# Kernel tuning notes

Measured on AMD Instinct MI355X. Metric: run time of the kernel, lower is better.

Reference implementation:

```python
import jax, jax.numpy as jnp
import numpy as np

FS = 3        # filter_size
STRIDE = 2
UPPER_PAD = 1
D_MODEL = 512


def setup_inputs() -> dict:
    key = jax.random.key(0)
    k1, k2, k3, k4 = jax.random.split(key, 4)
    b, h, n, d = 4, 8, 2048, D_MODEL
    nc = n // STRIDE
    layer_query = jax.random.normal(k1, (b, h, n, d), dtype=jnp.float32)
    uncompress_in = jax.random.normal(k2, (b, h, nc, d), dtype=jnp.float32)
    # nn.Linear(d*FS, d): weight (d, d*FS), bias (d,)
    W = jax.random.normal(k3, (d, d * FS), dtype=jnp.float32) * 0.02
    bias = jax.random.normal(k4, (d,), dtype=jnp.float32) * 0.01
    return {"layer_query": layer_query, "uncompress_in": uncompress_in,
            "W": W, "bias": bias, "i": 0}


def reference(layer_query, uncompress_in, W, bias, i):
    b, h, n, d = layer_query.shape
    # einsum('ijac,b->ijcab', u, kron_kernel) with kernel=[1,0,...] followed by
    # flatten(-2,-1) == transpose to (b,h,d,nc) then zero-upsample by STRIDE.
    u = jnp.swapaxes(uncompress_in, -1, -2)                      # (b,h,d,nc)
    nc = u.shape[-1]
    t = jnp.zeros(u.shape + (STRIDE,), u.dtype).at[..., 0].set(u)
    t = t.reshape(b, h, d, nc * STRIDE)                          # (b,h,d,nc*S)
    pad = FS - UPPER_PAD - 1
    t = jnp.pad(t, ((0, 0), (0, 0), (0, 0), (pad, pad)))
    # unfold(-1, FS, 1) then keep first n windows: window w covers t[..., w:w+FS]
    windows = jnp.stack([t[..., k:k + n] for k in range(FS)], axis=-1)  # (b,h,d,n,FS)
    up = jnp.transpose(windows, (0, 1, 3, 4, 2))                 # (b,h,n,FS,d)
    res_connect = up.sum(axis=3) / FS                            # (b,h,n,d)
    flat = up.reshape(b, h, n, FS * d)                           # (b,h,n,FS*d)
    out = jax.nn.relu(jnp.einsum('bhnk,dk->bhnd', flat, W) + bias)
    # dropout p=0.0 -> identity
    return layer_query + out + res_connect
```

## Files before the change

kernel.cpp:

```cpp
#include <hip/hip_runtime.h>
#include <cstdint>

#define NC    1024
#define D     512
#define KTOT  512
#define MTOT  32768
#define BK    64

typedef short  short8  __attribute__((ext_vector_type(8)));
typedef float  floatx4 __attribute__((ext_vector_type(4)));

__device__ inline void gl2lds16(const void* gptr, void* lptr) {
  __builtin_amdgcn_global_load_lds(
      (const __attribute__((address_space(1))) void*)gptr,
      (__attribute__((address_space(3))) void*)lptr,
      16, 0, 0);
}

__device__ inline unsigned short f2bf_rne(float f) {
  union { float f; unsigned u; } x; x.f = f;
  unsigned r = x.u + 0x7fffu + ((x.u >> 16) & 1u);
  return (unsigned short)(r >> 16);
}

__global__ __launch_bounds__(256) void cvt_f32_bf16_all(
    const float* __restrict__ srcU, unsigned short* __restrict__ dstU, int n4U,
    const float* __restrict__ srcW, unsigned short* __restrict__ dstW, int n4W) {
  int i = blockIdx.x * 256 + threadIdx.x;
  const float* src;
  unsigned short* dst;
  int idx;
  if (i < n4U) {
    src = srcU; dst = dstU; idx = i;
  } else {
    idx = i - n4U;
    if (idx >= n4W) return;
    src = srcW; dst = dstW;
  }
  float4 v = ((const float4*)src)[idx];
  ushort4 o;
  o.x = f2bf_rne(v.x); o.y = f2bf_rne(v.y);
  o.z = f2bf_rne(v.z); o.w = f2bf_rne(v.w);
  ((ushort4*)dst)[idx] = o;
}

__global__ __launch_bounds__(256, 2) void fused_uncompress_gemm(
    const unsigned short* __restrict__ Ub,
    const unsigned short* __restrict__ Wb,
    const float* __restrict__ U32,
    const float* __restrict__ LQ,
    const float* __restrict__ bias,
    float* __restrict__ out)
{
  __shared__ __attribute__((aligned(16))) unsigned char smem[129*128 + 192*128];
  unsigned char* smemA = smem;
  unsigned char* smemB = smem + 129*128;

  const int bid   = blockIdx.x;
  const int tileM = ((bid >> 6) << 3) | (bid & 7);
  const int tileN = (bid >> 3) & 7;
  const int r0 = tileM * 128;
  const int n0 = tileN * 64;
  const int tid  = threadIdx.x;
  const int wv   = tid >> 6;
  const int ln   = tid & 63;
  const int quad = ln >> 4;
  const int am   = ln & 15;

  floatx4 acc[2][12];
  #pragma unroll
  for (int rt = 0; rt < 2; ++rt)
    #pragma unroll
    for (int ct = 0; ct < 12; ++ct)
      acc[rt][ct] = floatx4{0.f, 0.f, 0.f, 0.f};

  const bool zeroExtra = (((r0 + 128) & (NC - 1)) == 0);

  for (int kc = 0; kc < KTOT / BK; ++kc) {
    const int k0 = kc * BK;

    #pragma unroll
    for (int i = 0; i < 4; ++i) {
      int row = wv * 32 + i * 8 + (ln >> 3);
      int s   = ln & 7;
      int kch = s ^ (row & 7);
      const unsigned short* g = Ub + (size_t)(r0 + row) * KTOT + k0 + kch * 8;
      gl2lds16(g, smemA + (wv * 32 + i * 8) * 128);
    }
    if (wv == 0 && ln < 8) {
      if (zeroExtra) {
        *(float4*)(smemA + 128 * 128 + ln * 16) = make_float4(0.f, 0.f, 0.f, 0.f);
      } else {
        const unsigned short* g = Ub + (size_t)(r0 + 128) * KTOT + k0 + ln * 8;
        gl2lds16(g, smemA + 128 * 128);
      }
    }
    #pragma unroll
    for (int i = 0; i < 6; ++i) {
      int rho = wv * 48 + i * 8 + (ln >> 3);
      int s   = ln & 7;
      int kch = s ^ (rho & 7);
      int beta = rho >> 6;
      int nl   = rho & 63;
      const unsigned short* g =
          Wb + (size_t)(n0 + nl) * 1536 + beta * 512 + k0 + kch * 8;
      gl2lds16(g, smemB + (wv * 48 + i * 8) * 128);
    }
    __syncthreads();

    #pragma unroll
    for (int ks = 0; ks < 2; ++ks) {
      short8 a0[2], a1[2];
      #pragma unroll
      for (int rt = 0; rt < 2; ++rt) {
        int row  = wv * 32 + rt * 16 + am;
        int sl   = (ks * 4 + quad) ^ (row & 7);
        a0[rt] = *(const short8*)(smemA + row * 128 + sl * 16);
        int row1 = row + 1;
        int sl1  = (ks * 4 + quad) ^ (row1 & 7);
        a1[rt] = *(const short8*)(smemA + row1 * 128 + sl1 * 16);
      }
      #pragma unroll
      for (int ct = 0; ct < 12; ++ct) {
        int beta = ct >> 2;
        int nl   = (ct & 3) * 16 + am;
        int rho  = beta * 64 + nl;
        int sl   = (ks * 4 + quad) ^ (nl & 7);
        short8 b = *(const short8*)(smemB + rho * 128 + sl * 16);
        #pragma unroll
        for (int rt = 0; rt < 2; ++rt) {
          acc[rt][ct] = __builtin_amdgcn_mfma_f32_16x16x32_bf16(
              (beta == 2) ? a1[rt] : a0[rt], b, acc[rt][ct], 0, 0, 0);
        }
      }
    }
    __syncthreads();
  }

  const float inv3 = 1.0f / 3.0f;
  float* Ew = (float*)smem + (size_t)wv * 2 * 16 * 68;
  float* Ow = Ew + 16 * 68;

  #pragma unroll
  for (int rt = 0; rt < 2; ++rt) {
    #pragma unroll
    for (int dt = 0; dt < 4; ++dt) {
      float bv = bias[n0 + dt * 16 + am];
      #pragma unroll
      for (int r = 0; r < 4; ++r) {
        int row16 = quad * 4 + r;
        float p0 = acc[rt][dt][r];
        float p1 = acc[rt][4 + dt][r];
        float p2 = acc[rt][8 + dt][r];
        Ew[row16 * 68 + dt * 16 + am] = fmaxf(p1 + bv, 0.f);
        Ow[row16 * 68 + dt * 16 + am] = fmaxf(p0 + p2 + bv, 0.f);
      }
    }
    #pragma unroll
    for (int rr = 0; rr < 4; ++rr) {
      int row16 = rr * 4 + quad;
      int jl = wv * 32 + rt * 16 + row16;
      int j  = r0 + jl;
      int head = j >> 10;
      int jn   = j & (NC - 1);
      float4 ev = *(const float4*)(Ew + row16 * 68 + am * 4);
      float4 ov = *(const float4*)(Ow + row16 * 68 + am * 4);
      size_t ucol = (size_t)j * D + n0 + am * 4;
      float4 u0 = *(const float4*)(U32 + ucol);
      float4 u1 = make_float4(0.f, 0.f, 0.f, 0.f);
      if (jn != NC - 1) u1 = *(const float4*)(U32 + ucol + D);
      size_t ob = ((size_t)head * 2048 + 2 * jn) * D + n0 + am * 4;
      float4 lq0 = *(const float4*)(LQ + ob);
      float4 lq1 = *(const float4*)(LQ + ob + D);
      float4 o0, o1;
      o0.x = lq0.x + ev.x + u0.x * inv3;
      o0.y = lq0.y + ev.y + u0.y * inv3;
      o0.z = lq0.z + ev.z + u0.z * inv3;
      o0.w = lq0.w + ev.w + u0.w * inv3;
      o1.x = lq1.x + ov.x + (u0.x + u1.x) * inv3;
      o1.y = lq1.y + ov.y + (u0.y + u1.y) * inv3;
      o1.z = lq1.z + ov.z + (u0.z + u1.z) * inv3;
      o1.w = lq1.w + ov.w + (u0.w + u1.w) * inv3;
      *(float4*)(out + ob)     = o0;
      *(float4*)(out + ob + D) = o1;
    }
  }
}

extern "C" void kernel_launch(void* const* d_in, const int* in_sizes, int n_in,
                              void* d_out, int out_size, void* d_ws, size_t ws_size,
                              hipStream_t stream) {
  const float* LQ   = (const float*)d_in[0];
  const float* U32  = (const float*)d_in[1];
  const float* W    = (const float*)d_in[2];
  const float* bias = (const float*)d_in[3];
  float* out = (float*)d_out;

  unsigned short* Ub = (unsigned short*)d_ws;
  unsigned short* Wb = (unsigned short*)((char*)d_ws + (size_t)MTOT * KTOT * 2);

  const int n4U = MTOT * KTOT / 4;
  const int n4W = 512 * 1536 / 4;
  cvt_f32_bf16_all<<<(n4U + n4W + 255) / 256, 256, 0, stream>>>(
      U32, Ub, n4U, W, Wb, n4W);

  fused_uncompress_gemm<<<dim3(2048), dim3(256), 0, stream>>>(
      Ub, Wb, U32, LQ, bias, out);
}
```

Before: 325.5 us.

## Double-buffer LDS tiles with BK=32 to overlap global loads with MFMA

Halves the K chunk to 32 and splits LDS into two buffers so the next chunk's global-to-LDS loads are issued before computing on the current chunk. This removes one barrier per iteration and is meant to hide load latency behind MFMA work. The swizzle changes to a 4-way XOR for 64-byte rows, and the zero row for sequence-boundary tiles is written once up front. The trade-off is twice as many iterations, each with less work per sync, and a narrower swizzle that may cause more LDS bank conflicts. LDS footprint stays about the same.

New measurement: 321.0 us. Within noise of the previous version (-1.4%).

```diff
diff --git a/kernel.cpp b/kernel.cpp
--- a/kernel.cpp
+++ b/kernel.cpp
@@ -5,7 +5,11 @@
 #define D     512
 #define KTOT  512
 #define MTOT  32768
-#define BK    64
+#define BK    32
+#define NKC   16
+#define ABYTES (129 * 64)
+#define BBYTES (192 * 64)
+#define BUFB   (ABYTES + BBYTES)
 
 typedef short  short8  __attribute__((ext_vector_type(8)));
 typedef float  floatx4 __attribute__((ext_vector_type(4)));
@@ -52,9 +56,7 @@
     const float* __restrict__ bias,
     float* __restrict__ out)
 {
-  __shared__ __attribute__((aligned(16))) unsigned char smem[129*128 + 192*128];
-  unsigned char* smemA = smem;
-  unsigned char* smemB = smem + 129*128;
+  __shared__ __attribute__((aligned(16))) unsigned char smem[2 * BUFB];
 
   const int bid   = blockIdx.x;
   const int tileM = ((bid >> 6) << 3) | (bid & 7);
@@ -76,62 +78,68 @@
 
   const bool zeroExtra = (((r0 + 128) & (NC - 1)) == 0);
 
-  for (int kc = 0; kc < KTOT / BK; ++kc) {
+  auto stage = [&](int buf, int kc) {
+    unsigned char* sA = smem + buf * BUFB;
+    unsigned char* sB = sA + ABYTES;
     const int k0 = kc * BK;
-
-    #pragma unroll
-    for (int i = 0; i < 4; ++i) {
-      int row = wv * 32 + i * 8 + (ln >> 3);
-      int s   = ln & 7;
-      int kch = s ^ (row & 7);
+    #pragma unroll
+    for (int i = 0; i < 2; ++i) {
+      int row = wv * 32 + i * 16 + (ln >> 2);
+      int kch = (ln & 3) ^ (row & 3);
       const unsigned short* g = Ub + (size_t)(r0 + row) * KTOT + k0 + kch * 8;
-      gl2lds16(g, smemA + (wv * 32 + i * 8) * 128);
-    }
-    if (wv == 0 && ln < 8) {
-      if (zeroExtra) {
-        *(float4*)(smemA + 128 * 128 + ln * 16) = make_float4(0.f, 0.f, 0.f, 0.f);
-      } else {
-        const unsigned short* g = Ub + (size_t)(r0 + 128) * KTOT + k0 + ln * 8;
-        gl2lds16(g, smemA + 128 * 128);
-      }
-    }
-    #pragma unroll
-    for (int i = 0; i < 6; ++i) {
-      int rho = wv * 48 + i * 8 + (ln >> 3);
-      int s   = ln & 7;
-      int kch = s ^ (rho & 7);
+      gl2lds16(g, sA + (wv * 32 + i * 16) * 64);
+    }
+    if (!zeroExtra && wv == 0 && ln < 4) {
+      const unsigned short* g = Ub + (size_t)(r0 + 128) * KTOT + k0 + ln * 8;
+      gl2lds16(g, sA + 128 * 64);
+    }
+    #pragma unroll
+    for (int i = 0; i < 3; ++i) {
+      int rho = wv * 48 + i * 16 + (ln >> 2);
+      int kch = (ln & 3) ^ (rho & 3);
       int beta = rho >> 6;
       int nl   = rho & 63;
       const unsigned short* g =
           Wb + (size_t)(n0 + nl) * 1536 + beta * 512 + k0 + kch * 8;
-      gl2lds16(g, smemB + (wv * 48 + i * 8) * 128);
-    }
-    __syncthreads();
-
-    #pragma unroll
-    for (int ks = 0; ks < 2; ++ks) {
-      short8 a0[2], a1[2];
+      gl2lds16(g, sB + (wv * 48 + i * 16) * 64);
+    }
+  };
+
+  if (zeroExtra && wv == 0 && ln < 4) {
+    *(float4*)(smem + ABYTES - 64 + ln * 16)        = make_float4(0.f, 0.f, 0.f, 0.f);
+    *(float4*)(smem + BUFB + ABYTES - 64 + ln * 16) = make_float4(0.f, 0.f, 0.f, 0.f);
+  }
+  stage(0, 0);
+  __syncthreads();
+
+  #pragma unroll 2
+  for (int kc = 0; kc < NKC; ++kc) {
+    const int cur = kc & 1;
+    if (kc < NKC - 1) stage(cur ^ 1, kc + 1);
+
+    unsigned char* sA = smem + cur * BUFB;
+    unsigned char* sB = sA + ABYTES;
+    short8 a0[2], a1[2];
+    #pragma unroll
+    for (int rt = 0; rt < 2; ++rt) {
+      int row  = wv * 32 + rt * 16 + am;
+      int sl   = quad ^ (row & 3);
+      a0[rt] = *(const short8*)(sA + row * 64 + sl * 16);
+      int row1 = row + 1;
+      int sl1  = quad ^ (row1 & 3);
+      a1[rt] = *(const short8*)(sA + row1 * 64 + sl1 * 16);
+    }
+    #pragma unroll
+    for (int ct = 0; ct < 12; ++ct) {
+      int beta = ct >> 2;
+      int nl   = (ct & 3) * 16 + am;
+      int rho  = beta * 64 + nl;
+      int sl   = quad ^ (rho & 3);
+      short8 b = *(const short8*)(sB + rho * 64 + sl * 16);
       #pragma unroll
       for (int rt = 0; rt < 2; ++rt) {
-        int row  = wv * 32 + rt * 16 + am;
-        int sl   = (ks * 4 + quad) ^ (row & 7);
-        a0[rt] = *(const short8*)(smemA + row * 128 + sl * 16);
-        int row1 = row + 1;
-        int sl1  = (ks * 4 + quad) ^ (row1 & 7);
-        a1[rt] = *(const short8*)(smemA + row1 * 128 + sl1 * 16);
-      }
-      #pragma unroll
-      for (int ct = 0; ct < 12; ++ct) {
-        int beta = ct >> 2;
-        int nl   = (ct & 3) * 16 + am;
-        int rho  = beta * 64 + nl;
-        int sl   = (ks * 4 + quad) ^ (nl & 7);
-        short8 b = *(const short8*)(smemB + rho * 128 + sl * 16);
-        #pragma unroll
-        for (int rt = 0; rt < 2; ++rt) {
-          acc[rt][ct] = __builtin_amdgcn_mfma_f32_16x16x32_bf16(
-              (beta == 2) ? a1[rt] : a0[rt], b, acc[rt][ct], 0, 0, 0);
-        }
+        acc[rt][ct] = __builtin_amdgcn_mfma_f32_16x16x32_bf16(
+            (beta == 2) ? a1[rt] : a0[rt], b, acc[rt][ct], 0, 0, 0);
       }
     }
     __syncthreads();
```
